# Optimization experiments

Measured on AMD Instinct MI355X. Metric: run time of the kernel, lower is better.

Reference implementation:

```python
import jax, jax.numpy as jnp
import numpy as np

K = 16  # neighbors

def setup_inputs() -> dict:
    key = jax.random.key(0)
    k1, k2, k3 = jax.random.split(key, 3)
    B, C_in, C_out, N = 4, 64, 64, 8192
    x = jax.random.normal(k1, (B, C_in, N), dtype=jnp.float32)
    coords = jax.random.normal(k2, (B, 3, N), dtype=jnp.float32)
    W = jax.random.normal(k3, (C_out, C_in), dtype=jnp.float32) * 0.05
    return {"x": x, "coords": coords, "W": W}


def _knn_indices(coords, k):
    # coords: [B, 3, N]; squared pairwise distances d[b,i,j] = ||c_i - c_j||^2
    sq = jnp.sum(coords * coords, axis=1)                      # [B, N]
    inner = jnp.einsum('bdi,bdj->bij', coords, coords)         # [B, N, N]
    dist = sq[:, :, None] + sq[:, None, :] - 2.0 * inner       # [B, N, N]
    # k smallest distances -> top_k of negated distances
    _, idx = jax.lax.top_k(-dist, k)                           # [B, N, k]
    return idx


def _gather_neighbors(x, idx):
    # x: [B, C, N], idx: [B, N, k] -> [B, C, N, k]
    return jax.vmap(lambda xb, ib: xb[:, ib])(x, idx)


def reference(x, coords, W):
    idx = _knn_indices(coords, K)                              # [B, N, k]
    knn_x = _gather_neighbors(x, idx)                          # [B, C_in, N, k]
    # PointwiseConv2D (1x1 conv, no bias) == channel matmul
    mlp = jnp.einsum('oc,bcnk->bonk', W, knn_x)                # [B, C_out, N, k]
    y = jnp.max(mlp, axis=-1)                                  # [B, C_out, N]
    return (y, coords)
```

## Files before the change

### kernel.cpp

```cpp
#include <hip/hip_runtime.h>

#define BB 4
#define NN 8192
#define QB 32
#define NW 8
#define CAP 96
#define SLACK 6e-3f

typedef unsigned long long u64;
typedef unsigned int u32;
typedef _Float16 f16x8 __attribute__((ext_vector_type(8)));
typedef float f32x16 __attribute__((ext_vector_type(16)));

__device__ __forceinline__ u64 shfl_xor_u64(u64 v, int m) {
  u32 lo = (u32)v, hi = (u32)(v >> 32);
  lo = (u32)__shfl_xor((int)lo, m, 64);
  hi = (u32)__shfl_xor((int)hi, m, 64);
  return ((u64)hi << 32) | lo;
}
__device__ __forceinline__ u64 shfl_u64(u64 v, int src) {
  u32 lo = (u32)v, hi = (u32)(v >> 32);
  lo = (u32)__shfl((int)lo, src, 64);
  hi = (u32)__shfl((int)hi, src, 64);
  return ((u64)hi << 32) | lo;
}
__device__ __forceinline__ u64 min_u64(u64 a, u64 b) { return a < b ? a : b; }
__device__ __forceinline__ float rfl(float x) {
  return __int_as_float(__builtin_amdgcn_readfirstlane(__float_as_int(x)));
}

__device__ __forceinline__ u64 bitonic64(u64 v, int lane) {
#pragma unroll
  for (int k = 2; k <= 64; k <<= 1) {
#pragma unroll
    for (int jm = k >> 1; jm >= 1; jm >>= 1) {
      u64 o = shfl_xor_u64(v, jm);
      bool keepmin = ((lane & jm) == 0) == ((lane & k) == 0);
      u64 mn = min_u64(v, o);
      u64 mx = (v < o) ? o : v;
      v = keepmin ? mn : mx;
    }
  }
  return v;
}

__device__ __forceinline__ u32 bitonic32v(u32 v, int lane) {
#pragma unroll
  for (int k = 2; k <= 64; k <<= 1) {
#pragma unroll
    for (int jm = k >> 1; jm >= 1; jm >>= 1) {
      u32 o = (u32)__shfl_xor((int)v, jm, 64);
      bool keepmin = ((lane & jm) == 0) == ((lane & k) == 0);
      v = keepmin ? (v < o ? v : o) : (v < o ? o : v);
    }
  }
  return v;
}

__device__ __forceinline__ float dist_exact(float qx, float qy, float qz, float qw,
                                            float cx, float cy, float cz, float cw) {
#pragma clang fp contract(off)
  float inner = qx * cx;
  inner = inner + qy * cy;
  inner = inner + qz * cz;
  float tt = qw + cw;
  return __builtin_fmaf(-2.0f, inner, tt);
}

__global__ void __launch_bounds__(256, 4) fused_prep_zmat(
    const float* __restrict__ x, const float* __restrict__ W,
    const float* __restrict__ coords,
    float* __restrict__ z, float4* __restrict__ c4p,
    _Float16* __restrict__ bfr,
    float* __restrict__ ycoords) {
#pragma clang fp contract(off)
  __shared__ float Wst[64 * 68];
  __shared__ float xs[64 * 64];
  int t = threadIdx.x;
  if (blockIdx.x < 512) {
    int blk = blockIdx.x;
    int b = blk >> 7;
    int j0 = (blk & 127) * 64;
    for (int r = t; r < 4096; r += 256) Wst[(r & 63) * 68 + (r >> 6)] = W[r];
    const float* xb = x + (size_t)b * 64 * NN;
#pragma unroll
    for (int r = 0; r < 16; ++r) {
      int idx = t + r * 256;
      int c = idx >> 6, j = idx & 63;
      xs[c * 64 + j] = xb[(size_t)c * NN + j0 + j];
    }
    __syncthreads();
    int o0 = (t & 15) * 4, jb = (t >> 4) * 4;
    float4 a0 = {0.f, 0.f, 0.f, 0.f}, a1 = a0, a2 = a0, a3 = a0;
#pragma unroll 4
    for (int c = 0; c < 64; ++c) {
      float4 w4 = *(const float4*)&Wst[c * 68 + o0];
      float4 x4 = *(const float4*)&xs[c * 64 + jb];
      a0.x = __builtin_fmaf(w4.x, x4.x, a0.x);
      a0.y = __builtin_fmaf(w4.y, x4.x, a0.y);
      a0.z = __builtin_fmaf(w4.z, x4.x, a0.z);
      a0.w = __builtin_fmaf(w4.w, x4.x, a0.w);
      a1.x = __builtin_fmaf(w4.x, x4.y, a1.x);
      a1.y = __builtin_fmaf(w4.y, x4.y, a1.y);
      a1.z = __builtin_fmaf(w4.z, x4.y, a1.z);
      a1.w = __builtin_fmaf(w4.w, x4.y, a1.w);
      a2.x = __builtin_fmaf(w4.x, x4.z, a2.x);
      a2.y = __builtin_fmaf(w4.y, x4.z, a2.y);
      a2.z = __builtin_fmaf(w4.z, x4.z, a2.z);
      a2.w = __builtin_fmaf(w4.w, x4.z, a2.w);
      a3.x = __builtin_fmaf(w4.x, x4.w, a3.x);
      a3.y = __builtin_fmaf(w4.y, x4.w, a3.y);
      a3.z = __builtin_fmaf(w4.z, x4.w, a3.z);
      a3.w = __builtin_fmaf(w4.w, x4.w, a3.w);
    }
    size_t rbase = (size_t)b * NN + j0 + jb;
    *(float4*)&z[(rbase + 0) * 64 + o0] = a0;
    *(float4*)&z[(rbase + 1) * 64 + o0] = a1;
    *(float4*)&z[(rbase + 2) * 64 + o0] = a2;
    *(float4*)&z[(rbase + 3) * 64 + o0] = a3;
  } else {
    int t2 = (blockIdx.x - 512) * 256 + t;
    int b = t2 >> 13;
    int i = t2 & (NN - 1);
    const float* cb = coords + (size_t)b * 3 * NN;
    float cx = cb[i];
    float cy = cb[NN + i];
    float cz = cb[2 * NN + i];
    float sq = (cx * cx + cy * cy) + cz * cz;
    float4 v; v.x = -2.0f * cx; v.y = -2.0f * cy; v.z = -2.0f * cz; v.w = sq;
    c4p[t2] = v;

    _Float16 xh = (_Float16)v.x, yh = (_Float16)v.y, zh = (_Float16)v.z;
    _Float16 xl = (_Float16)(v.x - (float)xh);
    _Float16 yl = (_Float16)(v.y - (float)yh);
    _Float16 zl = (_Float16)(v.z - (float)zh);
    _Float16 sh = (_Float16)sq;
    _Float16 sl = (_Float16)(sq - (float)sh);
    f16x8 b0, b1;
    b0[0] = xh; b0[1] = xh; b0[2] = xl; b0[3] = yh;
    b0[4] = yh; b0[5] = yl; b0[6] = zh; b0[7] = zh;
    b1[0] = zl; b1[1] = sh; b1[2] = sl;
    b1[3] = (_Float16)0.f; b1[4] = (_Float16)0.f; b1[5] = (_Float16)0.f;
    b1[6] = (_Float16)0.f; b1[7] = (_Float16)0.f;
    f16x8* bp = (f16x8*)bfr;
    bp[(size_t)t2 * 2]     = b0;
    bp[(size_t)t2 * 2 + 1] = b1;

#pragma unroll
    for (int r = 0; r < 3; ++r)
      ycoords[r * (BB * NN) + t2] = coords[r * (BB * NN) + t2];
  }
}

__global__ void __launch_bounds__(512, 8) knn_gather(const float4* __restrict__ c4p,
                                                     const _Float16* __restrict__ bfr,
                                                     const float* __restrict__ z,
                                                     float* __restrict__ y) {
  __shared__ __align__(16) char pool[QB * 128 * 4];
  __shared__ float TfL[QB];
  __shared__ int scnt[QB];
  __shared__ int sidx[QB][16];
  __shared__ float ys[64][QB + 1];
  float (*wmin)[128] = (float(*)[128])pool;
  u32 (*survj)[CAP] = (u32(*)[CAP])pool;

  int t = threadIdx.x;
  int w = t >> 6, lane = t & 63;
  int lq = lane & 31, lg = lane >> 5;
  int lg4 = lg << 2;
  int qbase = blockIdx.x * QB;
  int b = qbase >> 13;
  int i0 = qbase & (NN - 1);
  const float4* cp = c4p + (size_t)b * NN;
  int wbase = w * (NN / NW);

  if (t < QB) scnt[t] = 0;

  float4 qv = cp[i0 + lq];
  float qx = -0.5f * qv.x, qy = -0.5f * qv.y, qz = -0.5f * qv.z;
  _Float16 xh = (_Float16)qx, yh = (_Float16)qy, zh = (_Float16)qz;
  _Float16 xl = (_Float16)(qx - (float)xh);
  _Float16 yl = (_Float16)(qy - (float)yh);
  _Float16 zl = (_Float16)(qz - (float)zh);
  f16x8 af;
  if (lg == 0) {
    af[0] = xh; af[1] = xl; af[2] = xh; af[3] = yh;
    af[4] = yl; af[5] = yh; af[6] = zh; af[7] = zl;
  } else {
    af[0] = zh; af[1] = (_Float16)1.0f; af[2] = (_Float16)1.0f;
    af[3] = (_Float16)0.f; af[4] = (_Float16)0.f; af[5] = (_Float16)0.f;
    af[6] = (_Float16)0.f; af[7] = (_Float16)0.f;
  }

  f32x16 zzz, mn;
#pragma unroll
  for (int r = 0; r < 16; ++r) { zzz[r] = 0.f; mn[r] = 3.402823466e+38f; }

  const f16x8* lp = (const f16x8*)bfr + (((size_t)b * NN + wbase + lq) * 2 + lg);

#pragma unroll 2
  for (int tt = 0; tt < 32; tt += 2) {
    f16x8 bc0 = lp[tt * 64];
    f16x8 bc1 = lp[(tt + 1) * 64];
    f32x16 d0 = __builtin_amdgcn_mfma_f32_32x32x16_f16(af, bc0, zzz, 0, 0, 0);
    f32x16 d1 = __builtin_amdgcn_mfma_f32_32x32x16_f16(af, bc1, zzz, 0, 0, 0);
#pragma unroll
    for (int r = 0; r < 16; ++r) mn[r] = fminf(fminf(mn[r], d0[r]), d1[r]);
  }

#pragma unroll
  for (int r = 0; r < 16; ++r) {
    float m2 = fminf(mn[r], __shfl_xor(mn[r], 16, 64));
    int q = (r & 3) + 8 * (r >> 2) + lg4;
    if (lq < 16) wmin[q][w * 16 + lq] = m2;
  }
  __syncthreads();

#pragma unroll
  for (int qi = 0; qi < QB / NW; ++qi) {
    int q = w * (QB / NW) + qi;
    float v = fminf(wmin[q][2 * lane], wmin[q][2 * lane + 1]);
#pragma unroll
    for (int k = 2; k <= 64; k <<= 1) {
#pragma unroll
      for (int jm = k >> 1; jm >= 1; jm >>= 1) {
        float o = __shfl_xor(v, jm, 64);
        bool keepmin = ((lane & jm) == 0) == ((lane & k) == 0);
        v = keepmin ? fminf(v, o) : fmaxf(v, o);
      }
    }
    if (lane == 15) TfL[q] = v + SLACK;
  }
  __syncthreads();

  f32x16 mc;
#pragma unroll
  for (int r = 0; r < 16; ++r) mc[r] = -TfL[(r & 3) + 8 * (r >> 2) + lg4];

#pragma unroll 4
  for (int tt = 0; tt < 32; ++tt) {
    f16x8 bc = lp[tt * 64];
    f32x16 d = __builtin_amdgcn_mfma_f32_32x32x16_f16(af, bc, mc, 0, 0, 0);
    int cand = wbase + tt * 32 + lq;
#pragma unroll
    for (int r = 0; r < 16; ++r) {
      if (d[r] <= 0.f) {
        int q = (r & 3) + 8 * (r >> 2) + lg4;
        int pos = atomicAdd(&scnt[q], 1);
        if (pos < CAP) survj[q][pos] = (u32)cand;
      }
    }
  }
  __syncthreads();

  const float* zb = z + (size_t)b * NN * 64;
#pragma unroll 1
  for (int qi = 0; qi < QB / NW; ++qi) {
    int q = w * (QB / NW) + qi;
    int n = scnt[q]; if (n > CAP) n = CAP;
    float4 qq = cp[i0 + q];
    float eqx = rfl(-0.5f * qq.x), eqy = rfl(-0.5f * qq.y);
    float eqz = rfl(-0.5f * qq.z), eqw = rfl(qq.w);
    u32 m32 = 0xFFFFFFFFu, idxv = 0u;
    if (lane < n) {
      int c = (int)survj[q][lane];
      float4 cj = cp[c];
      float de = dist_exact(eqx, eqy, eqz, eqw,
                            -0.5f * cj.x, -0.5f * cj.y, -0.5f * cj.z, cj.w);
      u32 f = __float_as_uint(de);
      m32 = f ^ ((u32)(((int)f) >> 31) | 0x80000000u);
      idxv = (u32)c;
    }
    u32 T15 = (u32)__shfl((int)bitonic32v(m32, lane), 15, 64);
    u64 blt = __ballot(m32 < T15);
    u64 beq = __ballot(m32 == T15);
    int k2 = 16 - __popcll(blt);
    if (n <= 64 && __popcll(beq) == k2) {
      u64 sel = blt | beq;
      if ((sel >> lane) & 1ull) {
        int slot = __builtin_amdgcn_mbcnt_hi(
            (u32)(sel >> 32), __builtin_amdgcn_mbcnt_lo((u32)sel, 0u));
        sidx[q][slot] = (int)idxv;
      }
    } else {
      u64 v = (lane < n) ? (((u64)m32 << 32) | idxv) : ~0ull;
      v = bitonic64(v, lane);
      if (n > 64) {
        u64 v2 = ~0ull;
        if (lane + 64 < n) {
          int c = (int)survj[q][lane + 64];
          float4 cj = cp[c];
          float de = dist_exact(eqx, eqy, eqz, eqw,
                                -0.5f * cj.x, -0.5f * cj.y, -0.5f * cj.z, cj.w);
          u32 f = __float_as_uint(de);
          u32 mm = f ^ ((u32)(((int)f) >> 31) | 0x80000000u);
          v2 = ((u64)mm << 32) | (u32)c;
        }
        v2 = bitonic64(v2, lane);
        u64 s2 = shfl_u64(v2, (lane + 48) & 63);
        u64 vm = (lane < 16) ? v : ((lane < 32) ? s2 : ~0ull);
        v = bitonic64(vm, lane);
      }
      if (lane < 16) sidx[q][lane] = (int)(v & 0xFFFFFFFFull);
    }
  }

#pragma unroll 2
  for (int qi = 0; qi < QB / NW; ++qi) {
    int q = w * (QB / NW) + qi;
    const int* id = sidx[q];
    float vv[16];
#pragma unroll
    for (int k = 0; k < 16; ++k)
      vv[k] = zb[(size_t)id[k] * 64 + lane];
#pragma unroll
    for (int s = 8; s >= 1; s >>= 1)
#pragma unroll
      for (int k = 0; k < s; ++k) vv[k] = fmaxf(vv[k], vv[k + s]);
    ys[lane][q] = vv[0];
  }
  __syncthreads();
  {
    int o = t >> 3;
    int ql0 = (t & 7) * 4;
    float4 vv;
    vv.x = ys[o][ql0]; vv.y = ys[o][ql0 + 1];
    vv.z = ys[o][ql0 + 2]; vv.w = ys[o][ql0 + 3];
    *(float4*)&y[((size_t)b * 64 + o) * NN + i0 + ql0] = vv;
  }
}

extern "C" void kernel_launch(void* const* d_in, const int* in_sizes, int n_in,
                              void* d_out, int out_size, void* d_ws, size_t ws_size,
                              hipStream_t stream) {
  const float* x      = (const float*)d_in[0];
  const float* coords = (const float*)d_in[1];
  const float* W      = (const float*)d_in[2];
  float* y = (float*)d_out;

  char* ws = (char*)d_ws;
  float4*   c4p = (float4*)ws;
  _Float16* bfr = (_Float16*)(ws + (512u << 10));
  float*    z   = (float*)(ws + (2u << 20));

  float* ycoords = y + (size_t)BB * 64 * NN;

  fused_prep_zmat<<<512 + 128, 256, 0, stream>>>(x, W, coords, z, c4p, bfr, ycoords);
  knn_gather<<<BB * NN / QB, 512, 0, stream>>>(c4p, bfr, z, y);
}
```

Measured before the change: 130.3 us.

## Pack two queries per wavefront for top-16 selection and pair-test candidate filter

The per-query exact top-16 selection now handles two queries at once in the two 32-lane halves of the wavefront whenever both have at most 32 survivors, using a 32-wide bitonic sort on 64-bit keys. Queries with more survivors fall back to the older 64-wide sort, and the 32-bit threshold-and-ballot fast path is removed. The candidate filter after the MFMA first tests the min of each pair of distances, skipping two compares when both fail. The aim is to halve the serial selection passes, at the cost of a full 64-bit sort even in cases the old ballot path handled more cheaply.

```diff
diff --git a/kernel.cpp b/kernel.cpp
--- a/kernel.cpp
+++ b/kernel.cpp
@@ -39,19 +39,6 @@
       u64 mn = min_u64(v, o);
       u64 mx = (v < o) ? o : v;
       v = keepmin ? mn : mx;
-    }
-  }
-  return v;
-}
-
-__device__ __forceinline__ u32 bitonic32v(u32 v, int lane) {
-#pragma unroll
-  for (int k = 2; k <= 64; k <<= 1) {
-#pragma unroll
-    for (int jm = k >> 1; jm >= 1; jm >>= 1) {
-      u32 o = (u32)__shfl_xor((int)v, jm, 64);
-      bool keepmin = ((lane & jm) == 0) == ((lane & k) == 0);
-      v = keepmin ? (v < o ? v : o) : (v < o ? o : v);
     }
   }
   return v;
@@ -243,65 +230,93 @@
     f32x16 d = __builtin_amdgcn_mfma_f32_32x32x16_f16(af, bc, mc, 0, 0, 0);
     int cand = wbase + tt * 32 + lq;
 #pragma unroll
-    for (int r = 0; r < 16; ++r) {
-      if (d[r] <= 0.f) {
-        int q = (r & 3) + 8 * (r >> 2) + lg4;
-        int pos = atomicAdd(&scnt[q], 1);
-        if (pos < CAP) survj[q][pos] = (u32)cand;
+    for (int rp = 0; rp < 8; ++rp) {
+      float dm = fminf(d[2 * rp], d[2 * rp + 1]);
+      if (dm <= 0.f) {
+#pragma unroll
+        for (int rr = 0; rr < 2; ++rr) {
+          int r = 2 * rp + rr;
+          if (d[r] <= 0.f) {
+            int q = (r & 3) + 8 * (r >> 2) + lg4;
+            int pos = atomicAdd(&scnt[q], 1);
+            if (pos < CAP) survj[q][pos] = (u32)cand;
+          }
+        }
       }
     }
   }
   __syncthreads();
 
   const float* zb = z + (size_t)b * NN * 64;
+  int ll = lane & 31;
 #pragma unroll 1
-  for (int qi = 0; qi < QB / NW; ++qi) {
-    int q = w * (QB / NW) + qi;
-    int n = scnt[q]; if (n > CAP) n = CAP;
-    float4 qq = cp[i0 + q];
-    float eqx = rfl(-0.5f * qq.x), eqy = rfl(-0.5f * qq.y);
-    float eqz = rfl(-0.5f * qq.z), eqw = rfl(qq.w);
-    u32 m32 = 0xFFFFFFFFu, idxv = 0u;
-    if (lane < n) {
-      int c = (int)survj[q][lane];
-      float4 cj = cp[c];
-      float de = dist_exact(eqx, eqy, eqz, eqw,
-                            -0.5f * cj.x, -0.5f * cj.y, -0.5f * cj.z, cj.w);
-      u32 f = __float_as_uint(de);
-      m32 = f ^ ((u32)(((int)f) >> 31) | 0x80000000u);
-      idxv = (u32)c;
-    }
-    u32 T15 = (u32)__shfl((int)bitonic32v(m32, lane), 15, 64);
-    u64 blt = __ballot(m32 < T15);
-    u64 beq = __ballot(m32 == T15);
-    int k2 = 16 - __popcll(blt);
-    if (n <= 64 && __popcll(beq) == k2) {
-      u64 sel = blt | beq;
-      if ((sel >> lane) & 1ull) {
-        int slot = __builtin_amdgcn_mbcnt_hi(
-            (u32)(sel >> 32), __builtin_amdgcn_mbcnt_lo((u32)sel, 0u));
-        sidx[q][slot] = (int)idxv;
-      }
+  for (int qp = 0; qp < 2; ++qp) {
+    int qa = w * 4 + qp * 2, qb2 = qa + 1;
+    int na = scnt[qa]; if (na > CAP) na = CAP;
+    int nb = scnt[qb2]; if (nb > CAP) nb = CAP;
+    if (na <= 32 && nb <= 32) {
+      int qh = (lane < 32) ? qa : qb2;
+      int nh = (lane < 32) ? na : nb;
+      u64 v = ~0ull;
+      if (ll < nh) {
+        int c = (int)survj[qh][ll];
+        float4 qq = cp[i0 + qh];
+        float4 cj = cp[c];
+        float de = dist_exact(-0.5f * qq.x, -0.5f * qq.y, -0.5f * qq.z, qq.w,
+                              -0.5f * cj.x, -0.5f * cj.y, -0.5f * cj.z, cj.w);
+        u32 f = __float_as_uint(de);
+        u32 m32 = f ^ ((u32)(((int)f) >> 31) | 0x80000000u);
+        v = ((u64)m32 << 32) | (u32)c;
+      }
+#pragma unroll
+      for (int k = 2; k <= 32; k <<= 1) {
+#pragma unroll
+        for (int jm = k >> 1; jm >= 1; jm >>= 1) {
+          u64 o = shfl_xor_u64(v, jm);
+          bool keepmin = ((ll & jm) == 0) == ((ll & k) == 0);
+          u64 mn2 = min_u64(v, o);
+          u64 mx2 = (v < o) ? o : v;
+          v = keepmin ? mn2 : mx2;
+        }
+      }
+      if (ll < 16) sidx[qh][ll] = (int)(v & 0xFFFFFFFFull);
     } else {
-      u64 v = (lane < n) ? (((u64)m32 << 32) | idxv) : ~0ull;
-      v = bitonic64(v, lane);
-      if (n > 64) {
-        u64 v2 = ~0ull;
-        if (lane + 64 < n) {
-          int c = (int)survj[q][lane + 64];
+#pragma unroll 1
+      for (int qi2 = 0; qi2 < 2; ++qi2) {
+        int q = qa + qi2;
+        int n = scnt[q]; if (n > CAP) n = CAP;
+        float4 qq = cp[i0 + q];
+        float eqx = rfl(-0.5f * qq.x), eqy = rfl(-0.5f * qq.y);
+        float eqz = rfl(-0.5f * qq.z), eqw = rfl(qq.w);
+        u64 v = ~0ull;
+        if (lane < n) {
+          int c = (int)survj[q][lane];
           float4 cj = cp[c];
           float de = dist_exact(eqx, eqy, eqz, eqw,
                                 -0.5f * cj.x, -0.5f * cj.y, -0.5f * cj.z, cj.w);
           u32 f = __float_as_uint(de);
-          u32 mm = f ^ ((u32)(((int)f) >> 31) | 0x80000000u);
-          v2 = ((u64)mm << 32) | (u32)c;
+          u32 m32 = f ^ ((u32)(((int)f) >> 31) | 0x80000000u);
+          v = ((u64)m32 << 32) | (u32)c;
         }
-        v2 = bitonic64(v2, lane);
-        u64 s2 = shfl_u64(v2, (lane + 48) & 63);
-        u64 vm = (lane < 16) ? v : ((lane < 32) ? s2 : ~0ull);
-        v = bitonic64(vm, lane);
-      }
-      if (lane < 16) sidx[q][lane] = (int)(v & 0xFFFFFFFFull);
+        v = bitonic64(v, lane);
+        if (n > 64) {
+          u64 v2 = ~0ull;
+          if (lane + 64 < n) {
+            int c = (int)survj[q][lane + 64];
+            float4 cj = cp[c];
+            float de = dist_exact(eqx, eqy, eqz, eqw,
+                                  -0.5f * cj.x, -0.5f * cj.y, -0.5f * cj.z, cj.w);
+            u32 f = __float_as_uint(de);
+            u32 mm = f ^ ((u32)(((int)f) >> 31) | 0x80000000u);
+            v2 = ((u64)mm << 32) | (u32)c;
+          }
+          v2 = bitonic64(v2, lane);
+          u64 s2 = shfl_u64(v2, (lane + 48) & 63);
+          u64 vm = (lane < 16) ? v : ((lane < 32) ? s2 : ~0ull);
+          v = bitonic64(vm, lane);
+        }
+        if (lane < 16) sidx[q][lane] = (int)(v & 0xFFFFFFFFull);
+      }
     }
   }
 
```

New measurement: 134.8 us. 1.03x slower.
